# Kernel tuning notes

Measured on AMD Instinct MI355X. Metric: run time of the kernel, lower is better.

The kernel has to match this reference:

```python
import jax, jax.numpy as jnp
import numpy as np

N_HEADS = 2
WINDOW = 4
BLOCK = 256


def _get_rel_emb(emb, length):
    # emb: [1, 2*WINDOW+1, K] -> [1, 2*length-1, K]
    pad = max(length - (WINDOW + 1), 0)
    start = max((WINDOW + 1) - length, 0)
    e = jnp.pad(emb, ((0, 0), (pad, pad), (0, 0)))
    return e[:, start:start + 2 * length - 1]


def _rel_to_abs(x):
    # x: [b, h, l, 2l-1] -> [b, h, l, l] (skew trick)
    b, h, l, _ = x.shape
    x = jnp.pad(x, ((0, 0), (0, 0), (0, 0), (0, 1))).reshape(b, h, 2 * l * l)
    x = jnp.pad(x, ((0, 0), (0, 0), (0, l - 1))).reshape(b, h, l + 1, 2 * l - 1)
    return x[:, :, :l, l - 1:]


def _abs_to_rel(x):
    # x: [b, h, l, l] -> [b, h, l, 2l-1] (inverse skew)
    b, h, l, _ = x.shape
    x = jnp.pad(x, ((0, 0), (0, 0), (0, 0), (0, l - 1))).reshape(b, h, l * (2 * l - 1))
    x = jnp.pad(x, ((0, 0), (0, 0), (l, 0))).reshape(b, h, l, 2 * l)
    return x[:, :, :, 1:]


def _attention(x, c, attn_mask, Wq, bq, Wk, bk, Wv, bv, Wo, bo, emb_rel_k, emb_rel_v):
    B, C, T = x.shape
    H, K = N_HEADS, C // N_HEADS
    # projections (torch Linear on [B,T,C])
    q = (jnp.einsum('bct,cd->btd', x, Wq) + bq).reshape(B, T, H, K).transpose(0, 2, 1, 3)
    k = (jnp.einsum('bct,cd->btd', c, Wk) + bk).reshape(B, T, H, K).transpose(0, 2, 1, 3)
    v = (jnp.einsum('bct,cd->btd', c, Wv) + bv).reshape(B, T, H, K).transpose(0, 2, 1, 3)
    qs = q / jnp.sqrt(jnp.float32(K))
    scores = jnp.einsum('bhtk,bhsk->bhts', qs, k)  # [B,H,T,T]
    # relative-position key logits (heads_share=True -> single table)
    rel_k = _get_rel_emb(emb_rel_k, T)[0]          # [2T-1, K]
    rel_logits = jnp.einsum('bhtk,rk->bhtr', qs, rel_k)
    scores = scores + _rel_to_abs(rel_logits)
    # proximal bias: -log1p(|i-j|)
    r = jnp.arange(T, dtype=jnp.float32)
    scores = scores - jnp.log1p(jnp.abs(r[:, None] - r[None, :]))[None, None]
    # attn mask + block-local mask (block mask active because mask is given)
    ij = jnp.arange(T)
    block_ok = jnp.abs(ij[:, None] - ij[None, :]) <= BLOCK
    valid = (attn_mask != 0) & block_ok[None, None]
    scores = jnp.where(valid, scores, jnp.float32(-1e4))
    p = jax.nn.softmax(scores, axis=-1)
    out = jnp.einsum('bhts,bhsk->bhtk', p, v)
    # relative-position value contribution
    rel_v = _get_rel_emb(emb_rel_v, T)[0]          # [2T-1, K]
    out = out + jnp.einsum('bhtr,rk->bhtk', _abs_to_rel(p), rel_v)
    out = out.transpose(0, 2, 1, 3).reshape(B, T, C)
    y = jnp.einsum('btd,do->bto', out, Wo) + bo
    return y.transpose(0, 2, 1)  # [B, out_channels, T]


def setup_inputs() -> dict:
    key = jax.random.key(0)
    ks = jax.random.split(key, 8)
    B, C, T = 4, 192, 2048
    K = C // N_HEADS
    s = jnp.float32(0.05)
    rel_std = jnp.float32(K ** -0.5)
    return {
        'x': jax.random.normal(ks[0], (B, C, T), jnp.float32),
        'c': jax.random.normal(ks[1], (B, C, T), jnp.float32),
        'Wq': jax.random.normal(ks[2], (C, C), jnp.float32) * s,
        'bq': jnp.zeros((C,), jnp.float32),
        'Wk': jax.random.normal(ks[3], (C, C), jnp.float32) * s,
        'bk': jnp.zeros((C,), jnp.float32),
        'Wv': jax.random.normal(ks[4], (C, C), jnp.float32) * s,
        'bv': jnp.zeros((C,), jnp.float32),
        'Wo': jax.random.normal(ks[5], (C, C), jnp.float32) * s,
        'bo': jnp.zeros((C,), jnp.float32),
        'emb_rel_k': jax.random.normal(ks[6], (1, 2 * WINDOW + 1, K), jnp.float32) * rel_std,
        'emb_rel_v': jax.random.normal(ks[7], (1, 2 * WINDOW + 1, K), jnp.float32) * rel_std,
        'attn_mask': jnp.ones((B, 1, T, T), jnp.int32),
    }


def reference(x, c, Wq, bq, Wk, bk, Wv, bv, Wo, bo, emb_rel_k, emb_rel_v, attn_mask):
    return _attention(x, c, attn_mask, Wq, bq, Wk, bk, Wv, bv, Wo, bo, emb_rel_k, emb_rel_v)
```

## Files before the change

### kernel.cpp

```cpp
#include <hip/hip_runtime.h>
#include <hip/hip_bf16.h>

#define B_DIM 4
#define C_DIM 192
#define T_SEQ 2048
#define H_DIM 2
#define K_DIM 96
#define BAND 256
#define IT 16
#define WSLOT 544
#define W_P 548
#define PMW 17

typedef __attribute__((ext_vector_type(8))) short bf16x8;
typedef __attribute__((ext_vector_type(4))) short bf16x4;
typedef __attribute__((ext_vector_type(4))) float f32x4;
#define MFMA16 __builtin_amdgcn_mfma_f32_16x16x32_bf16

__device__ __forceinline__ float bfbits2f(short s) {
    union { short s; __hip_bfloat16 h; } u; u.s = s; return __bfloat162float(u.h);
}
__device__ __forceinline__ short f2bf_bits(float f) {
    union { __hip_bfloat16 h; short s; } u; u.h = __float2bfloat16(f); return u.s;
}

#define OFF_WT(m)  ((size_t)(m)*73728)
#define OFF_BQS    ((size_t)294912)
#define OFF_RELKBF ((size_t)295680)
#define OFF_PM     ((size_t)298752)
#define OFF_QBF    ((size_t)855808)
#define OFF_KBF    (OFF_QBF + 3145728)
#define OFF_VTB    (OFF_KBF + 3145728)
#define OFF_OBTC   (OFF_VTB + 3145728)

__global__ __launch_bounds__(256)
void prep_kernel(const float* __restrict__ Wq, const float* __restrict__ Wk,
                 const float* __restrict__ Wv, const float* __restrict__ Wo,
                 const float* __restrict__ bq, const float* __restrict__ relk,
                 const int* __restrict__ mask, char* __restrict__ ws)
{
    const float qscale = 0.10206207261596577f;
    const int bidx = blockIdx.x;
    const int tid  = threadIdx.x;

    if (bidx < 576) {
        const size_t idx = (size_t)bidx*256 + tid;
        const int mi  = (int)(idx / 36864);
        const int rem = (int)(idx % 36864);
        const int c = rem / C_DIM, d = rem % C_DIM;
        const float* src = (mi == 0) ? Wq : (mi == 1) ? Wk : (mi == 2) ? Wv : Wo;
        float v = src[c*C_DIM + d];
        if (mi == 0) v *= qscale;
        ((short*)(ws + OFF_WT(mi)))[d*C_DIM + c] = f2bf_bits(v);
        return;
    }
    if (bidx < 1120) {
        const int idx = (bidx - 576)*256 + tid;
        const int b = idx / (T_SEQ*PMW);
        const int rem = idx % (T_SEQ*PMW);
        const int i = rem / PMW, w = rem % PMW;
        const int jlo = max(0, (i & ~15) - BAND);
        const int* mrow = mask + ((size_t)b*T_SEQ + i)*T_SEQ;
        unsigned bits = 0;
        #pragma unroll
        for (int g4 = 0; g4 < 8; ++g4) {
            const int jg = jlo + 32*w + 4*g4;
            if (jg + 3 < T_SEQ) {
                const int4 mv = *reinterpret_cast<const int4*>(mrow + jg);
                bits |= (unsigned)(mv.x != 0) << (4*g4);
                bits |= (unsigned)(mv.y != 0) << (4*g4+1);
                bits |= (unsigned)(mv.z != 0) << (4*g4+2);
                bits |= (unsigned)(mv.w != 0) << (4*g4+3);
            } else {
                #pragma unroll
                for (int e = 0; e < 4; ++e)
                    if (jg + e < T_SEQ && mrow[jg+e] != 0) bits |= 1u << (4*g4+e);
            }
        }
        ((unsigned*)(ws + OFF_PM))[idx] = bits;
        return;
    }
    if (tid < C_DIM)
        ((float*)(ws + OFF_BQS))[tid] = bq[tid]*qscale;
    short* rkb = (short*)(ws + OFF_RELKBF);
    for (int idx = tid; idx < 16*K_DIM; idx += 256) {
        const int row = idx / K_DIM;
        rkb[idx] = (row < 9) ? f2bf_bits(relk[idx]) : (short)0;
    }
}

__global__ __launch_bounds__(256)
void proj_kernel(const float* __restrict__ x, const float* __restrict__ cin,
                 const float* __restrict__ bk, const float* __restrict__ bv,
                 char* __restrict__ ws)
{
    __shared__ short xs[IT*C_DIM];
    __shared__ short cs[IT*C_DIM];
    const int b   = blockIdx.x >> 7;
    const int t0  = (blockIdx.x & 127) * IT;
    const int tid = threadIdx.x;
    const int wave = tid >> 6, lane = tid & 63;
    const int q4 = lane >> 4, lr = lane & 15;

    for (int l = tid; l < 768; l += 256) {
        const int cr = l >> 2, u = l & 3;
        const size_t off = (size_t)(b*C_DIM + cr)*T_SEQ + t0 + 4*u;
        const float4 xv = *reinterpret_cast<const float4*>(x + off);
        const float4 cv = *reinterpret_cast<const float4*>(cin + off);
        xs[(4*u+0)*C_DIM + cr] = f2bf_bits(xv.x);
        xs[(4*u+1)*C_DIM + cr] = f2bf_bits(xv.y);
        xs[(4*u+2)*C_DIM + cr] = f2bf_bits(xv.z);
        xs[(4*u+3)*C_DIM + cr] = f2bf_bits(xv.w);
        cs[(4*u+0)*C_DIM + cr] = f2bf_bits(cv.x);
        cs[(4*u+1)*C_DIM + cr] = f2bf_bits(cv.y);
        cs[(4*u+2)*C_DIM + cr] = f2bf_bits(cv.z);
        cs[(4*u+3)*C_DIM + cr] = f2bf_bits(cv.w);
    }
    __syncthreads();

    const short* WqT = (const short*)(ws + OFF_WT(0));
    const short* WkT = (const short*)(ws + OFF_WT(1));
    const short* WvT = (const short*)(ws + OFF_WT(2));

    f32x4 qa[3], ka[3], va[3];
    #pragma unroll
    for (int j = 0; j < 3; ++j) {
        qa[j] = (f32x4){0,0,0,0}; ka[j] = (f32x4){0,0,0,0}; va[j] = (f32x4){0,0,0,0};
    }
    for (int kc = 0; kc < 6; ++kc) {
        const int ko = kc*32 + q4*8;
        const bf16x8 xf = *reinterpret_cast<const bf16x8*>(xs + lr*C_DIM + ko);
        const bf16x8 cf = *reinterpret_cast<const bf16x8*>(cs + lr*C_DIM + ko);
        #pragma unroll
        for (int j = 0; j < 3; ++j) {
            const int dt = 3*wave + j;
            const bf16x8 wqf = *reinterpret_cast<const bf16x8*>(WqT + (dt*16 + lr)*C_DIM + ko);
            const bf16x8 wkf = *reinterpret_cast<const bf16x8*>(WkT + (dt*16 + lr)*C_DIM + ko);
            const bf16x8 wvf = *reinterpret_cast<const bf16x8*>(WvT + (dt*16 + lr)*C_DIM + ko);
            qa[j] = MFMA16(xf, wqf, qa[j], 0, 0, 0);
            ka[j] = MFMA16(cf, wkf, ka[j], 0, 0, 0);
            va[j] = MFMA16(wvf, cf, va[j], 0, 0, 0);
        }
    }

    const float* bqs = (const float*)(ws + OFF_BQS);
    short* qbf = (short*)(ws + OFF_QBF);
    short* kbf = (short*)(ws + OFF_KBF);
    short* vtb = (short*)(ws + OFF_VTB);
    #pragma unroll
    for (int j = 0; j < 3; ++j) {
        const int dt = 3*wave + j;
        {
            const int d = dt*16 + lr, h = d/K_DIM, kk = d%K_DIM;
            const int bh = b*H_DIM + h;
            const float bq_v = bqs[d], bk_v = bk[d];
            #pragma unroll
            for (int e = 0; e < 4; ++e) {
                const int t = t0 + q4*4 + e;
                const size_t off = ((size_t)bh*T_SEQ + t)*K_DIM + kk;
                qbf[off] = f2bf_bits(qa[j][e] + bq_v);
                kbf[off] = f2bf_bits(ka[j][e] + bk_v);
            }
        }
        {
            #pragma unroll
            for (int e = 0; e < 4; ++e) {
                const int d = dt*16 + q4*4 + e, h = d/K_DIM, kk = d%K_DIM;
                const int bh = b*H_DIM + h;
                vtb[((size_t)bh*K_DIM + kk)*T_SEQ + t0 + lr] = f2bf_bits(va[j][e] + bv[d]);
            }
        }
    }
}

__global__ __launch_bounds__(256)
void attn_kernel(const float* __restrict__ relv, char* __restrict__ ws)
{
    __shared__ float p_s[IT*W_P];
    __shared__ float shbuf[864];

    const short* qbf = (const short*)(ws + OFF_QBF);
    const short* kbf = (const short*)(ws + OFF_KBF);
    const short* vtb = (const short*)(ws + OFF_VTB);
    const short* rkb = (const short*)(ws + OFF_RELKBF);
    const unsigned* pm = (const unsigned*)(ws + OFF_PM);
    short* obtc = (short*)(ws + OFF_OBTC);

    const int bh  = blockIdx.x >> 7;
    const int i0  = (blockIdx.x & 127) * IT;
    const int b   = bh / H_DIM;
    const int h   = bh % H_DIM;
    const int tid = threadIdx.x;
    const int wave = tid >> 6, lane = tid & 63;
    const int q4 = lane >> 4, lr = lane & 15;

    const int jlo  = max(0, i0 - BAND);
    const int jhi  = min(T_SEQ - 1, i0 + IT - 1 + BAND);
    const int wlen = jhi - jlo + 1;
    const size_t qkv_base = (size_t)bh * T_SEQ * K_DIM;

    float* lt = shbuf;
    float* rl = shbuf + 260;
    for (int idx = tid; idx < 257; idx += 256) lt[idx] = log1pf((float)idx);

    bf16x8 qa[3];
    {
        const short* qrow = qbf + qkv_base + (size_t)(i0 + lr)*K_DIM + q4*8;
        #pragma unroll
        for (int kc = 0; kc < 3; ++kc)
            qa[kc] = *reinterpret_cast<const bf16x8*>(qrow + kc*32);
    }

    for (int jt = wave; jt < WSLOT/16; jt += 4) {
        int jr = jlo + jt*16 + lr;
        if (jr > T_SEQ-1) jr = T_SEQ-1;
        const short* krow = kbf + qkv_base + (size_t)jr*K_DIM + q4*8;
        f32x4 s = {0.f,0.f,0.f,0.f};
        #pragma unroll
        for (int kc = 0; kc < 3; ++kc)
            s = MFMA16(qa[kc], *reinterpret_cast<const bf16x8*>(krow + kc*32), s, 0, 0, 0);
        #pragma unroll
        for (int e = 0; e < 4; ++e)
            p_s[(q4*4 + e)*W_P + jt*16 + lr] = s[e];
    }
    if (wave == 3) {
        const short* krow = rkb + lr*K_DIM + q4*8;
        f32x4 s = {0.f,0.f,0.f,0.f};
        #pragma unroll
        for (int kc = 0; kc < 3; ++kc)
            s = MFMA16(qa[kc], *reinterpret_cast<const bf16x8*>(krow + kc*32), s, 0, 0, 0);
        if (lr < 9) {
            #pragma unroll
            for (int e = 0; e < 4; ++e)
                rl[(q4*4 + e)*9 + lr] = s[e];
        }
    }
    __syncthreads();

    {
        const int r = tid >> 4, sj = tid & 15;
        const int i = i0 + r;
        const int pmrow = (b*T_SEQ + i)*PMW;
        float vals[36];
        float m = -INFINITY;
        #pragma unroll
        for (int mm = 0; mm < 9; ++mm) {
            const int j0 = 4*sj + 64*mm;
            float4 pv = make_float4(0.f,0.f,0.f,0.f);
            unsigned mb = 0;
            if (j0 < WSLOT) {
                pv = *reinterpret_cast<const float4*>(p_s + r*W_P + j0);
                mb = pm[pmrow + (j0 >> 5)] >> (j0 & 31);
            }
            const float pe[4] = {pv.x, pv.y, pv.z, pv.w};
            #pragma unroll
            for (int e = 0; e < 4; ++e) {
                const int j = j0 + e;
                float val = -INFINITY;
                if (j0 < WSLOT && j < wlen) {
                    const int jg = jlo + j, dd = jg - i;
                    const int ad = dd < 0 ? -dd : dd;
                    if (ad <= BAND && ((mb >> e) & 1)) {
                        val = pe[e] - lt[ad];
                        if ((unsigned)(dd + 4) <= 8u) val += rl[r*9 + dd + 4];
                    }
                }
                vals[mm*4 + e] = val;
                m = fmaxf(m, val);
            }
        }
        #pragma unroll
        for (int off = 8; off > 0; off >>= 1) m = fmaxf(m, __shfl_xor(m, off, 64));
        if (m == -INFINITY) m = 0.f;
        float ssum = 0.f;
        #pragma unroll
        for (int u = 0; u < 36; ++u) { vals[u] = __expf(vals[u] - m); ssum += vals[u]; }
        #pragma unroll
        for (int off = 8; off > 0; off >>= 1) ssum += __shfl_xor(ssum, off, 64);
        const float inv = ssum > 0.f ? 1.f/ssum : 0.f;
        short* pb = (short*)p_s;
        #pragma unroll
        for (int mm = 0; mm < 9; ++mm) {
            const int j0 = 4*sj + 64*mm;
            if (j0 < WSLOT) {
                bf16x4 w;
                #pragma unroll
                for (int e = 0; e < 4; ++e) w[e] = f2bf_bits(vals[mm*4+e]*inv);
                *reinterpret_cast<bf16x4*>(pb + r*(2*W_P) + j0) = w;
            }
        }
    }
    __syncthreads();

    for (int idx = tid; idx < 9*K_DIM; idx += 256) shbuf[idx] = relv[idx];

    const short* pb = (const short*)p_s;
    f32x4 o0 = {0.f,0.f,0.f,0.f}, o1 = {0.f,0.f,0.f,0.f};
    for (int kc = 0; kc < WSLOT/32; ++kc) {
        const bf16x8 pa = *reinterpret_cast<const bf16x8*>(pb + lr*(2*W_P) + kc*32 + q4*8);
        int tc = jlo + kc*32 + q4*8;
        if (tc > T_SEQ-8) tc = T_SEQ-8;
        const bf16x8 vb0 = *reinterpret_cast<const bf16x8*>(
            vtb + qkv_base + (size_t)(wave*16 + lr)*T_SEQ + tc);
        o0 = MFMA16(pa, vb0, o0, 0, 0, 0);
        if (wave < 2) {
            const bf16x8 vb1 = *reinterpret_cast<const bf16x8*>(
                vtb + qkv_base + (size_t)((wave+4)*16 + lr)*T_SEQ + tc);
            o1 = MFMA16(pa, vb1, o1, 0, 0, 0);
        }
    }
    __syncthreads();

    #pragma unroll
    for (int u = 0; u < 2; ++u) {
        if (u == 1 && wave >= 2) break;
        const int nt = (u == 0) ? wave : wave + 4;
        const f32x4 oc = (u == 0) ? o0 : o1;
        const int col = nt*16 + lr;
        #pragma unroll
        for (int e = 0; e < 4; ++e) {
            const int row = q4*4 + e;
            const int i = i0 + row;
            float v = oc[e];
            #pragma unroll
            for (int dd = 0; dd < 9; ++dd) {
                const int jg = i + dd - 4;
                if (jg >= 0 && jg < T_SEQ)
                    v += bfbits2f(pb[row*(2*W_P) + (jg - jlo)]) * shbuf[dd*K_DIM + col];
            }
            obtc[((size_t)b*T_SEQ + i)*C_DIM + h*K_DIM + col] = f2bf_bits(v);
        }
    }
}

__global__ __launch_bounds__(256)
void oproj_kernel(const float* __restrict__ bo, float* __restrict__ y,
                  const char* __restrict__ ws)
{
    const int b   = blockIdx.x >> 7;
    const int t0  = (blockIdx.x & 127) * 16;
    const int tid = threadIdx.x;
    const int wave = tid >> 6, lane = tid & 63;
    const int q4 = lane >> 4, lr = lane & 15;

    const short* WoT  = (const short*)(ws + OFF_WT(3));
    const short* obtc = (const short*)(ws + OFF_OBTC);

    f32x4 a[3];
    #pragma unroll
    for (int j = 0; j < 3; ++j) a[j] = (f32x4){0.f,0.f,0.f,0.f};
    for (int kc = 0; kc < 6; ++kc) {
        const int ko = kc*32 + q4*8;
        const bf16x8 bf = *reinterpret_cast<const bf16x8*>(
            obtc + ((size_t)b*T_SEQ + t0 + lr)*C_DIM + ko);
        #pragma unroll
        for (int j = 0; j < 3; ++j) {
            const bf16x8 af = *reinterpret_cast<const bf16x8*>(
                WoT + ((3*wave + j)*16 + lr)*C_DIM + ko);
            a[j] = MFMA16(af, bf, a[j], 0, 0, 0);
        }
    }
    #pragma unroll
    for (int j = 0; j < 3; ++j) {
        #pragma unroll
        for (int e = 0; e < 4; ++e) {
            const int d = (3*wave + j)*16 + q4*4 + e;
            y[((size_t)b*C_DIM + d)*T_SEQ + t0 + lr] = a[j][e] + bo[d];
        }
    }
}

extern "C" void kernel_launch(void* const* d_in, const int* in_sizes, int n_in,
                              void* d_out, int out_size, void* d_ws, size_t ws_size,
                              hipStream_t stream)
{
    const float* x    = (const float*)d_in[0];
    const float* c    = (const float*)d_in[1];
    const float* Wq   = (const float*)d_in[2];
    const float* bq   = (const float*)d_in[3];
    const float* Wk   = (const float*)d_in[4];
    const float* bk   = (const float*)d_in[5];
    const float* Wv   = (const float*)d_in[6];
    const float* bv   = (const float*)d_in[7];
    const float* Wo   = (const float*)d_in[8];
    const float* bo   = (const float*)d_in[9];
    const float* relk = (const float*)d_in[10];
    const float* relv = (const float*)d_in[11];
    const int*   mask = (const int*)d_in[12];
    float*       y    = (float*)d_out;
    char*        ws   = (char*)d_ws;

    hipLaunchKernelGGL(prep_kernel, dim3(1121), dim3(256), 0, stream,
                       Wq, Wk, Wv, Wo, bq, relk, mask, ws);
    hipLaunchKernelGGL(proj_kernel, dim3(B_DIM*(T_SEQ/16)), dim3(256), 0, stream,
                       x, c, bk, bv, ws);
    hipLaunchKernelGGL(attn_kernel, dim3(B_DIM*H_DIM*(T_SEQ/IT)), dim3(256), 0, stream,
                       relv, ws);
    hipLaunchKernelGGL(oproj_kernel, dim3(B_DIM*(T_SEQ/16)), dim3(256), 0, stream,
                       bo, y, ws);
}
```

Baseline: 179.5 us.

## Fuse attention with output projection, compute mask bits in-block, MFMA rel-value

Merges the attention and output-projection kernels into one 512-thread block that handles both heads for a 16-row tile, keeping the attention output in shared memory instead of writing it to a global bf16 buffer and reading it back. Mask bit-packing moves from the prep kernel into the attention block, so the packed mask no longer goes through global memory. The relative-value contribution now uses an MFMA against a transposed, zero-padded rel_v table rather than a scalar loop. The cost is fewer blocks (512 instead of 1024), larger shared-memory use per block, and one fewer kernel launch.

```diff
diff --git a/kernel.cpp b/kernel.cpp
--- a/kernel.cpp
+++ b/kernel.cpp
@@ -11,6 +11,8 @@
 #define WSLOT 544
 #define W_P 548
 #define PMW 17
+#define HSTR (IT*W_P)
+#define OSTR 200
 
 typedef __attribute__((ext_vector_type(8))) short bf16x8;
 typedef __attribute__((ext_vector_type(4))) short bf16x4;
@@ -27,17 +29,16 @@
 #define OFF_WT(m)  ((size_t)(m)*73728)
 #define OFF_BQS    ((size_t)294912)
 #define OFF_RELKBF ((size_t)295680)
-#define OFF_PM     ((size_t)298752)
-#define OFF_QBF    ((size_t)855808)
+#define OFF_RVT    ((size_t)298752)
+#define OFF_QBF    ((size_t)304896)
 #define OFF_KBF    (OFF_QBF + 3145728)
 #define OFF_VTB    (OFF_KBF + 3145728)
-#define OFF_OBTC   (OFF_VTB + 3145728)
 
 __global__ __launch_bounds__(256)
 void prep_kernel(const float* __restrict__ Wq, const float* __restrict__ Wk,
                  const float* __restrict__ Wv, const float* __restrict__ Wo,
                  const float* __restrict__ bq, const float* __restrict__ relk,
-                 const int* __restrict__ mask, char* __restrict__ ws)
+                 const float* __restrict__ relv, char* __restrict__ ws)
 {
     const float qscale = 0.10206207261596577f;
     const int bidx = blockIdx.x;
@@ -54,38 +55,17 @@
         ((short*)(ws + OFF_WT(mi)))[d*C_DIM + c] = f2bf_bits(v);
         return;
     }
-    if (bidx < 1120) {
-        const int idx = (bidx - 576)*256 + tid;
-        const int b = idx / (T_SEQ*PMW);
-        const int rem = idx % (T_SEQ*PMW);
-        const int i = rem / PMW, w = rem % PMW;
-        const int jlo = max(0, (i & ~15) - BAND);
-        const int* mrow = mask + ((size_t)b*T_SEQ + i)*T_SEQ;
-        unsigned bits = 0;
-        #pragma unroll
-        for (int g4 = 0; g4 < 8; ++g4) {
-            const int jg = jlo + 32*w + 4*g4;
-            if (jg + 3 < T_SEQ) {
-                const int4 mv = *reinterpret_cast<const int4*>(mrow + jg);
-                bits |= (unsigned)(mv.x != 0) << (4*g4);
-                bits |= (unsigned)(mv.y != 0) << (4*g4+1);
-                bits |= (unsigned)(mv.z != 0) << (4*g4+2);
-                bits |= (unsigned)(mv.w != 0) << (4*g4+3);
-            } else {
-                #pragma unroll
-                for (int e = 0; e < 4; ++e)
-                    if (jg + e < T_SEQ && mrow[jg+e] != 0) bits |= 1u << (4*g4+e);
-            }
-        }
-        ((unsigned*)(ws + OFF_PM))[idx] = bits;
-        return;
-    }
     if (tid < C_DIM)
         ((float*)(ws + OFF_BQS))[tid] = bq[tid]*qscale;
     short* rkb = (short*)(ws + OFF_RELKBF);
     for (int idx = tid; idx < 16*K_DIM; idx += 256) {
         const int row = idx / K_DIM;
         rkb[idx] = (row < 9) ? f2bf_bits(relk[idx]) : (short)0;
+    }
+    short* rvt = (short*)(ws + OFF_RVT);
+    for (int idx = tid; idx < K_DIM*32; idx += 256) {
+        const int col = idx >> 5, dd = idx & 31;
+        rvt[idx] = (dd < 9) ? f2bf_bits(relv[dd*K_DIM + col]) : (short)0;
     }
 }
 
@@ -173,57 +153,81 @@
     }
 }
 
-__global__ __launch_bounds__(256)
-void attn_kernel(const float* __restrict__ relv, char* __restrict__ ws)
+__global__ __launch_bounds__(512, 4)
+void attn_oproj_kernel(const int* __restrict__ mask, const float* __restrict__ bo,
+                       float* __restrict__ y, char* __restrict__ ws)
 {
-    __shared__ float p_s[IT*W_P];
-    __shared__ float shbuf[864];
+    __shared__ float ps[2*HSTR];
+    __shared__ float lt[257];
+    __shared__ float rl[2*144];
+    __shared__ unsigned pm_s[IT*PMW];
+    __shared__ short pd_s[2*IT*32];
 
     const short* qbf = (const short*)(ws + OFF_QBF);
     const short* kbf = (const short*)(ws + OFF_KBF);
     const short* vtb = (const short*)(ws + OFF_VTB);
     const short* rkb = (const short*)(ws + OFF_RELKBF);
-    const unsigned* pm = (const unsigned*)(ws + OFF_PM);
-    short* obtc = (short*)(ws + OFF_OBTC);
-
-    const int bh  = blockIdx.x >> 7;
+    const short* rvt = (const short*)(ws + OFF_RVT);
+    const short* WoT = (const short*)(ws + OFF_WT(3));
+
+    const int b   = blockIdx.x >> 7;
     const int i0  = (blockIdx.x & 127) * IT;
-    const int b   = bh / H_DIM;
-    const int h   = bh % H_DIM;
     const int tid = threadIdx.x;
     const int wave = tid >> 6, lane = tid & 63;
+    const int head = wave >> 2, wv = wave & 3;
     const int q4 = lane >> 4, lr = lane & 15;
 
     const int jlo  = max(0, i0 - BAND);
     const int jhi  = min(T_SEQ - 1, i0 + IT - 1 + BAND);
     const int wlen = jhi - jlo + 1;
-    const size_t qkv_base = (size_t)bh * T_SEQ * K_DIM;
-
-    float* lt = shbuf;
-    float* rl = shbuf + 260;
-    for (int idx = tid; idx < 257; idx += 256) lt[idx] = log1pf((float)idx);
+    const size_t qk_base = (size_t)(b*H_DIM + head) * T_SEQ * K_DIM;
+
+    for (int idx = tid; idx < 257; idx += 512) lt[idx] = log1pf((float)idx);
+
+    if (tid < IT*PMW) {
+        const int r = tid / PMW, w = tid % PMW;
+        const int* mrow = mask + ((size_t)b*T_SEQ + i0 + r)*T_SEQ;
+        unsigned bits = 0;
+        #pragma unroll
+        for (int g4 = 0; g4 < 8; ++g4) {
+            const int jg = jlo + 32*w + 4*g4;
+            if (jg + 3 < T_SEQ) {
+                const int4 mv = *reinterpret_cast<const int4*>(mrow + jg);
+                bits |= (unsigned)(mv.x != 0) << (4*g4);
+                bits |= (unsigned)(mv.y != 0) << (4*g4+1);
+                bits |= (unsigned)(mv.z != 0) << (4*g4+2);
+                bits |= (unsigned)(mv.w != 0) << (4*g4+3);
+            } else {
+                #pragma unroll
+                for (int e = 0; e < 4; ++e)
+                    if (jg + e < T_SEQ && mrow[jg+e] != 0) bits |= 1u << (4*g4+e);
+            }
+        }
+        pm_s[tid] = bits;
+    }
 
     bf16x8 qa[3];
     {
-        const short* qrow = qbf + qkv_base + (size_t)(i0 + lr)*K_DIM + q4*8;
+        const short* qrow = qbf + qk_base + (size_t)(i0 + lr)*K_DIM + q4*8;
         #pragma unroll
         for (int kc = 0; kc < 3; ++kc)
             qa[kc] = *reinterpret_cast<const bf16x8*>(qrow + kc*32);
     }
 
-    for (int jt = wave; jt < WSLOT/16; jt += 4) {
+    float* psh = ps + head*HSTR;
+    for (int jt = wv; jt < WSLOT/16; jt += 4) {
         int jr = jlo + jt*16 + lr;
         if (jr > T_SEQ-1) jr = T_SEQ-1;
-        const short* krow = kbf + qkv_base + (size_t)jr*K_DIM + q4*8;
+        const short* krow = kbf + qk_base + (size_t)jr*K_DIM + q4*8;
         f32x4 s = {0.f,0.f,0.f,0.f};
         #pragma unroll
         for (int kc = 0; kc < 3; ++kc)
             s = MFMA16(qa[kc], *reinterpret_cast<const bf16x8*>(krow + kc*32), s, 0, 0, 0);
         #pragma unroll
         for (int e = 0; e < 4; ++e)
-            p_s[(q4*4 + e)*W_P + jt*16 + lr] = s[e];
-    }
-    if (wave == 3) {
+            psh[(q4*4 + e)*W_P + jt*16 + lr] = s[e];
+    }
+    if (wv == 3) {
         const short* krow = rkb + lr*K_DIM + q4*8;
         f32x4 s = {0.f,0.f,0.f,0.f};
         #pragma unroll
@@ -232,15 +236,16 @@
         if (lr < 9) {
             #pragma unroll
             for (int e = 0; e < 4; ++e)
-                rl[(q4*4 + e)*9 + lr] = s[e];
+                rl[head*144 + (q4*4 + e)*9 + lr] = s[e];
         }
     }
     __syncthreads();
 
     {
-        const int r = tid >> 4, sj = tid & 15;
+        const int rg = tid >> 4, sj = tid & 15;
+        const int hh = rg >> 4, r = rg & 15;
         const int i = i0 + r;
-        const int pmrow = (b*T_SEQ + i)*PMW;
+        float* prow = ps + hh*HSTR + r*W_P;
         float vals[36];
         float m = -INFINITY;
         #pragma unroll
@@ -249,8 +254,8 @@
             float4 pv = make_float4(0.f,0.f,0.f,0.f);
             unsigned mb = 0;
             if (j0 < WSLOT) {
-                pv = *reinterpret_cast<const float4*>(p_s + r*W_P + j0);
-                mb = pm[pmrow + (j0 >> 5)] >> (j0 & 31);
+                pv = *reinterpret_cast<const float4*>(prow + j0);
+                mb = pm_s[r*PMW + (j0 >> 5)] >> (j0 & 31);
             }
             const float pe[4] = {pv.x, pv.y, pv.z, pv.w};
             #pragma unroll
@@ -262,7 +267,7 @@
                     const int ad = dd < 0 ? -dd : dd;
                     if (ad <= BAND && ((mb >> e) & 1)) {
                         val = pe[e] - lt[ad];
-                        if ((unsigned)(dd + 4) <= 8u) val += rl[r*9 + dd + 4];
+                        if ((unsigned)(dd + 4) <= 8u) val += rl[hh*144 + r*9 + dd + 4];
                     }
                 }
                 vals[mm*4 + e] = val;
@@ -278,7 +283,7 @@
         #pragma unroll
         for (int off = 8; off > 0; off >>= 1) ssum += __shfl_xor(ssum, off, 64);
         const float inv = ssum > 0.f ? 1.f/ssum : 0.f;
-        short* pb = (short*)p_s;
+        short* pbrow = (short*)prow;
         #pragma unroll
         for (int mm = 0; mm < 9; ++mm) {
             const int j0 = 4*sj + 64*mm;
@@ -286,86 +291,85 @@
                 bf16x4 w;
                 #pragma unroll
                 for (int e = 0; e < 4; ++e) w[e] = f2bf_bits(vals[mm*4+e]*inv);
-                *reinterpret_cast<bf16x4*>(pb + r*(2*W_P) + j0) = w;
+                *reinterpret_cast<bf16x4*>(pbrow + j0) = w;
             }
         }
     }
     __syncthreads();
 
-    for (int idx = tid; idx < 9*K_DIM; idx += 256) shbuf[idx] = relv[idx];
-
-    const short* pb = (const short*)p_s;
+    for (int idx = tid; idx < 2*IT*32; idx += 512) {
+        const int hh = idx >> 9, r = (idx >> 5) & 15, kk = idx & 31;
+        short v = 0;
+        if (kk < 9) {
+            const int jg = i0 + r + kk - 4;
+            if (jg >= 0 && jg < T_SEQ)
+                v = ((const short*)(ps + hh*HSTR))[r*(2*W_P) + (jg - jlo)];
+        }
+        pd_s[idx] = v;
+    }
+
+    const short* pbh = (const short*)(ps + head*HSTR);
     f32x4 o0 = {0.f,0.f,0.f,0.f}, o1 = {0.f,0.f,0.f,0.f};
     for (int kc = 0; kc < WSLOT/32; ++kc) {
-        const bf16x8 pa = *reinterpret_cast<const bf16x8*>(pb + lr*(2*W_P) + kc*32 + q4*8);
+        const bf16x8 pa = *reinterpret_cast<const bf16x8*>(pbh + lr*(2*W_P) + kc*32 + q4*8);
         int tc = jlo + kc*32 + q4*8;
         if (tc > T_SEQ-8) tc = T_SEQ-8;
         const bf16x8 vb0 = *reinterpret_cast<const bf16x8*>(
-            vtb + qkv_base + (size_t)(wave*16 + lr)*T_SEQ + tc);
+            vtb + qk_base + (size_t)(wv*16 + lr)*T_SEQ + tc);
         o0 = MFMA16(pa, vb0, o0, 0, 0, 0);
-        if (wave < 2) {
+        if (wv < 2) {
             const bf16x8 vb1 = *reinterpret_cast<const bf16x8*>(
-                vtb + qkv_base + (size_t)((wave+4)*16 + lr)*T_SEQ + tc);
+                vtb + qk_base + (size_t)((wv+4)*16 + lr)*T_SEQ + tc);
             o1 = MFMA16(pa, vb1, o1, 0, 0, 0);
         }
     }
     __syncthreads();
 
-    #pragma unroll
-    for (int u = 0; u < 2; ++u) {
-        if (u == 1 && wave >= 2) break;
-        const int nt = (u == 0) ? wave : wave + 4;
-        const f32x4 oc = (u == 0) ? o0 : o1;
-        const int col = nt*16 + lr;
-        #pragma unroll
-        for (int e = 0; e < 4; ++e) {
-            const int row = q4*4 + e;
-            const int i = i0 + row;
-            float v = oc[e];
-            #pragma unroll
-            for (int dd = 0; dd < 9; ++dd) {
-                const int jg = i + dd - 4;
-                if (jg >= 0 && jg < T_SEQ)
-                    v += bfbits2f(pb[row*(2*W_P) + (jg - jlo)]) * shbuf[dd*K_DIM + col];
-            }
-            obtc[((size_t)b*T_SEQ + i)*C_DIM + h*K_DIM + col] = f2bf_bits(v);
-        }
-    }
-}
-
-__global__ __launch_bounds__(256)
-void oproj_kernel(const float* __restrict__ bo, float* __restrict__ y,
-                  const char* __restrict__ ws)
-{
-    const int b   = blockIdx.x >> 7;
-    const int t0  = (blockIdx.x & 127) * 16;
-    const int tid = threadIdx.x;
-    const int wave = tid >> 6, lane = tid & 63;
-    const int q4 = lane >> 4, lr = lane & 15;
-
-    const short* WoT  = (const short*)(ws + OFF_WT(3));
-    const short* obtc = (const short*)(ws + OFF_OBTC);
-
-    f32x4 a[3];
-    #pragma unroll
-    for (int j = 0; j < 3; ++j) a[j] = (f32x4){0.f,0.f,0.f,0.f};
-    for (int kc = 0; kc < 6; ++kc) {
-        const int ko = kc*32 + q4*8;
-        const bf16x8 bf = *reinterpret_cast<const bf16x8*>(
-            obtc + ((size_t)b*T_SEQ + t0 + lr)*C_DIM + ko);
-        #pragma unroll
-        for (int j = 0; j < 3; ++j) {
-            const bf16x8 af = *reinterpret_cast<const bf16x8*>(
-                WoT + ((3*wave + j)*16 + lr)*C_DIM + ko);
-            a[j] = MFMA16(af, bf, a[j], 0, 0, 0);
-        }
-    }
-    #pragma unroll
-    for (int j = 0; j < 3; ++j) {
-        #pragma unroll
-        for (int e = 0; e < 4; ++e) {
-            const int d = (3*wave + j)*16 + q4*4 + e;
-            y[((size_t)b*C_DIM + d)*T_SEQ + t0 + lr] = a[j][e] + bo[d];
+    {
+        const bf16x8 pda = *reinterpret_cast<const bf16x8*>(pd_s + head*(IT*32) + lr*32 + q4*8);
+        const bf16x8 rv0 = *reinterpret_cast<const bf16x8*>(rvt + (wv*16 + lr)*32 + q4*8);
+        o0 = MFMA16(pda, rv0, o0, 0, 0, 0);
+        if (wv < 2) {
+            const bf16x8 rv1 = *reinterpret_cast<const bf16x8*>(rvt + ((wv+4)*16 + lr)*32 + q4*8);
+            o1 = MFMA16(pda, rv1, o1, 0, 0, 0);
+        }
+    }
+
+    {
+        short* outs = (short*)ps;
+        #pragma unroll
+        for (int u = 0; u < 2; ++u) {
+            if (u == 1 && wv >= 2) break;
+            const int nt = u ? wv + 4 : wv;
+            const f32x4 oc = u ? o1 : o0;
+            const int col = head*K_DIM + nt*16 + lr;
+            #pragma unroll
+            for (int e = 0; e < 4; ++e)
+                outs[(q4*4 + e)*OSTR + col] = f2bf_bits(oc[e]);
+        }
+    }
+    __syncthreads();
+
+    {
+        const short* outs = (const short*)ps;
+        #pragma unroll
+        for (int u = 0; u < 2; ++u) {
+            if (u == 1 && wave >= 4) break;
+            const int dt = u ? wave + 8 : wave;
+            f32x4 a = {0.f,0.f,0.f,0.f};
+            #pragma unroll
+            for (int kc = 0; kc < 6; ++kc) {
+                const int ko = kc*32 + q4*8;
+                const bf16x8 af = *reinterpret_cast<const bf16x8*>(
+                    WoT + (size_t)(dt*16 + lr)*C_DIM + ko);
+                const bf16x8 bfr = *reinterpret_cast<const bf16x8*>(outs + lr*OSTR + ko);
+                a = MFMA16(af, bfr, a, 0, 0, 0);
+            }
+            #pragma unroll
+            for (int e = 0; e < 4; ++e) {
+                const int d = dt*16 + q4*4 + e;
+                y[((size_t)b*C_DIM + d)*T_SEQ + i0 + lr] = a[e] + bo[d];
+            }
         }
     }
 }
@@ -390,12 +394,10 @@
     float*       y    = (float*)d_out;
     char*        ws   = (char*)d_ws;
 
-    hipLaunchKernelGGL(prep_kernel, dim3(1121), dim3(256), 0, stream,
-                       Wq, Wk, Wv, Wo, bq, relk, mask, ws);
+    hipLaunchKernelGGL(prep_kernel, dim3(577), dim3(256), 0, stream,
+                       Wq, Wk, Wv, Wo, bq, relk, relv, ws);
     hipLaunchKernelGGL(proj_kernel, dim3(B_DIM*(T_SEQ/16)), dim3(256), 0, stream,
                        x, c, bk, bv, ws);
-    hipLaunchKernelGGL(attn_kernel, dim3(B_DIM*H_DIM*(T_SEQ/IT)), dim3(256), 0, stream,
-                       relv, ws);
-    hipLaunchKernelGGL(oproj_kernel, dim3(B_DIM*(T_SEQ/16)), dim3(256), 0, stream,
-                       bo, y, ws);
-}
+    hipLaunchKernelGGL(attn_oproj_kernel, dim3(B_DIM*(T_SEQ/IT)), dim3(512), 0, stream,
+                       mask, bo, y, ws);
+}
```

Result: faster. 175.4 us (-2.3%).
